# Optimization experiments

Measured on AMD Instinct MI355X. Metric: run time of the kernel, lower is better.

## Reference

```python
import jax, jax.numpy as jnp
import numpy as np

FC = 8  # heads_count
EPS = 1e-12  # torch F.normalize eps


def setup_inputs() -> dict:
    key = jax.random.key(0)
    ks = jax.random.split(key, 8)
    n, l, s, C, H = 4, 4096, 256, 256, 256
    return {
        "x0": jax.random.normal(ks[0], (n, l, C), jnp.float32),
        "center1": jax.random.normal(ks[1], (n, s, C), jnp.float32),
        "W0": jax.random.normal(ks[2], (H, C), jnp.float32) * 0.05,
        "b0": jax.random.normal(ks[3], (H,), jnp.float32) * 0.05,
        "W1": jax.random.normal(ks[4], (2 * H, C), jnp.float32) * 0.05,
        "b1": jax.random.normal(ks[5], (2 * H,), jnp.float32) * 0.05,
        "Wm": jax.random.normal(ks[6], (C, H), jnp.float32) * 0.05,
        "bm": jax.random.normal(ks[7], (C,), jnp.float32) * 0.05,
        "alpha": jnp.ones((1,), jnp.float32),
        "beta": jnp.zeros((1,), jnp.float32),
    }


def _l2norm(x):
    # matches torch F.normalize(dim=-1): x / max(||x||, eps)
    nrm = jnp.sqrt(jnp.sum(x * x, axis=-1, keepdims=True))
    return x / jnp.maximum(nrm, EPS)


def reference(x0, center1, W0, b0, W1, b1, Wm, bm, alpha, beta):
    n, l, c = x0.shape
    s = center1.shape[1]
    H = W0.shape[0]
    sc = H // FC
    m = n * FC
    # projections
    x0p = x0 @ W0.T + b0                        # [n, l, H]
    c1 = center1 @ W1.T + b1                    # [n, s, 2H]
    # split heads: 'n l (fc sc) -> (n fc) l sc'
    x0p = x0p.reshape(n, l, FC, sc).transpose(0, 2, 1, 3).reshape(m, l, sc)
    c1 = c1.reshape(n, s, FC, 2 * sc).transpose(0, 2, 1, 3).reshape(m, s, 2 * sc)
    c_point, c_value = c1[..., :sc], c1[..., sc:]
    # cosine similarity + affine + sigmoid
    sim = jnp.einsum('mlc,msc->mls', _l2norm(x0p), _l2norm(c_point))
    sim = jax.nn.sigmoid(alpha[0] * sim + beta[0])
    # top-1 hard routing
    max_vals = jnp.max(sim, axis=2)             # [m, l]
    max_idx = jnp.argmax(sim, axis=2)           # [m, l]
    gathered = jnp.take_along_axis(c_value, max_idx[:, :, None], axis=1)  # [m, l, sc]
    dispatched = max_vals[:, :, None] * gathered
    # '(n fc) l sc -> n l (fc sc)'
    dispatched = dispatched.reshape(n, FC, l, sc).transpose(0, 2, 1, 3).reshape(n, l, H)
    return dispatched @ Wm.T + bm               # [n, l, c]
```

## Files before the change

### kernel.cpp

```cpp
#include <hip/hip_runtime.h>
#include <math.h>

#define Nn 4
#define Ll 4096
#define Ss 256
#define Cc 256
#define FC 8
#define SC 32

typedef __attribute__((ext_vector_type(8))) short short8;
typedef __attribute__((ext_vector_type(8))) _Float16 half8;
typedef __attribute__((ext_vector_type(4))) float f32x4;

__device__ __forceinline__ unsigned short f2bf(float x) {
  unsigned int u = __float_as_uint(x);
  return (unsigned short)((u + 0x7FFFu + ((u >> 16) & 1u)) >> 16);
}

__device__ __forceinline__ void split8v(float4 a, float4 b,
                                        half8& hi, half8& lo) {
  float v[8] = {a.x, a.y, a.z, a.w, b.x, b.y, b.z, b.w};
#pragma unroll
  for (int i = 0; i < 8; i++) {
    float x = v[i];
    _Float16 h = (_Float16)x;
    float r = (x - (float)h) * 2048.f;
    hi[i] = h;
    lo[i] = (_Float16)r;
  }
}

#define STAGE(Abuf, Bbuf, K0)                                               \
  {                                                                         \
    _Pragma("unroll")                                                       \
    for (int j = 0; j < 4; j++) {                                           \
      int c = wave * 4 + j;                                                 \
      const float* g = Ag + (m0blk + 8 * c + lr) * Cc + (K0) + scol;        \
      __builtin_amdgcn_global_load_lds(                                     \
          (const __attribute__((address_space(1))) void*)g,                 \
          (__attribute__((address_space(3))) void*)((Abuf) + c * 256),      \
          16, 0, 0);                                                        \
    }                                                                       \
    _Pragma("unroll")                                                       \
    for (int j = 0; j < 2; j++) {                                           \
      int c = wave * 2 + j;                                                 \
      const float* g =                                                      \
          Bg + (size_t)(n0blk + 8 * c + lr) * Cc + (K0) + scol;             \
      __builtin_amdgcn_global_load_lds(                                     \
          (const __attribute__((address_space(1))) void*)g,                 \
          (__attribute__((address_space(3))) void*)((Bbuf) + c * 256),      \
          16, 0, 0);                                                        \
    }                                                                       \
  }

#define KSTEP(Ac, Bc)                                                       \
  {                                                                         \
    half8 Bh[2], Bl[2];                                                     \
    _Pragma("unroll")                                                       \
    for (int ni = 0; ni < 2; ni++) {                                        \
      int rw = bR0 + ni * 16 + l15;                                         \
      int rb = rw * 32, xs = rw & 7;                                        \
      float4 f0 = *(const float4*)&(Bc)[rb + (((quad * 2) ^ xs) << 2)];     \
      float4 f1 = *(const float4*)&(Bc)[rb + (((quad * 2 + 1) ^ xs) << 2)]; \
      split8v(f0, f1, Bh[ni], Bl[ni]);                                      \
    }                                                                       \
    _Pragma("unroll")                                                       \
    for (int mi = 0; mi < 4; mi++) {                                        \
      int rw = aR0 + mi * 16 + l15;                                         \
      int rb = rw * 32, xs = rw & 7;                                        \
      float4 f0 = *(const float4*)&(Ac)[rb + (((quad * 2) ^ xs) << 2)];     \
      float4 f1 = *(const float4*)&(Ac)[rb + (((quad * 2 + 1) ^ xs) << 2)]; \
      half8 Ah, Al;                                                         \
      split8v(f0, f1, Ah, Al);                                              \
      _Pragma("unroll")                                                     \
      for (int ni = 0; ni < 2; ni++) {                                      \
        acc1[mi][ni] = __builtin_amdgcn_mfma_f32_16x16x32_f16(              \
            Ah, Bh[ni], acc1[mi][ni], 0, 0, 0);                             \
        acc2[mi][ni] = __builtin_amdgcn_mfma_f32_16x16x32_f16(              \
            Ah, Bl[ni], acc2[mi][ni], 0, 0, 0);                             \
        acc2[mi][ni] = __builtin_amdgcn_mfma_f32_16x16x32_f16(              \
            Al, Bh[ni], acc2[mi][ni], 0, 0, 0);                             \
      }                                                                     \
    }                                                                       \
  }

__global__ __launch_bounds__(256) void proj_mfma_k(
    const float* __restrict__ x0, const float* __restrict__ W0,
    const float* __restrict__ b0, const float* __restrict__ center1,
    const float* __restrict__ W1, const float* __restrict__ b1,
    float* __restrict__ xn, float* __restrict__ cpn, float* __restrict__ cval) {
  __shared__ float As[2][128 * 32];
  __shared__ float Bs[2][64 * 32];
  int t = threadIdx.x;
  int wave = t >> 6, lane = t & 63;
  int quad = lane >> 4, l15 = lane & 15;
  int l8 = lane & 7, lr = lane >> 3;
  int scol = (l8 ^ lr) << 2;
  int b = blockIdx.x;

  const float *Ag, *Bg, *bias;
  size_t m0blk;
  int n0blk;
  bool isX = (b < 512);
  if (isX) {
    int rt = b & 127, cb = b >> 7;
    m0blk = (size_t)rt * 128;
    n0blk = cb * 64;
    Ag = x0; Bg = W0; bias = b0;
  } else {
    int b2 = b - 512;
    m0blk = (size_t)(b2 >> 3) * 128;
    n0blk = (b2 & 7) * 64;
    Ag = center1; Bg = W1; bias = b1;
  }

  int n0w = n0blk + (wave >> 1) * 32;
  int aR0 = (wave & 1) * 64;
  int bR0 = (wave >> 1) * 32;

  f32x4 acc1[4][2], acc2[4][2];
#pragma unroll
  for (int ni = 0; ni < 2; ni++) {
    float bv = bias[n0w + ni * 16 + l15];
    f32x4 ci = {bv, bv, bv, bv};
    f32x4 zz = {0.f, 0.f, 0.f, 0.f};
#pragma unroll
    for (int mi = 0; mi < 4; mi++) { acc1[mi][ni] = ci; acc2[mi][ni] = zz; }
  }

  float* Ac = &As[0][0]; float* An = &As[1][0];
  float* Bc = &Bs[0][0]; float* Bn = &Bs[1][0];
  STAGE(Ac, Bc, 0);
#pragma unroll 1
  for (int kt = 0; kt < 8; kt++) {
    if (kt < 7) {
      STAGE(An, Bn, (kt + 1) * 32);
      asm volatile("s_waitcnt vmcnt(6)" ::: "memory");
    } else {
      asm volatile("s_waitcnt vmcnt(0)" ::: "memory");
    }
    __builtin_amdgcn_sched_barrier(0);
    __syncthreads();
    KSTEP(Ac, Bc);
    __syncthreads();
    float* tp;
    tp = Ac; Ac = An; An = tp;
    tp = Bc; Bc = Bn; Bn = tp;
  }

  if (isX) {
    size_t m0 = m0blk + aR0;
#pragma unroll
    for (int mi = 0; mi < 4; mi++) {
#pragma unroll
      for (int reg = 0; reg < 4; reg++) {
        size_t row = m0 + mi * 16 + quad * 4 + reg;
        float* orow = xn + row * Cc + n0w;
#pragma unroll
        for (int ni = 0; ni < 2; ni++)
          orow[ni * 16 + l15] =
              acc1[mi][ni][reg] + acc2[mi][ni][reg] * (1.f / 2048.f);
      }
    }
  } else {
    int f = n0w >> 6;
    bool point = (n0w & 32) == 0;
    int m0 = (int)m0blk + aR0;
#pragma unroll
    for (int mi = 0; mi < 4; mi++) {
#pragma unroll
      for (int reg = 0; reg < 4; reg++) {
        int row = m0 + mi * 16 + quad * 4 + reg;
        int nI = row >> 8, s = row & 255;
        float v0 = acc1[mi][0][reg] + acc2[mi][0][reg] * (1.f / 2048.f);
        float v1 = acc1[mi][1][reg] + acc2[mi][1][reg] * (1.f / 2048.f);
        size_t base = (((size_t)nI * FC + f) * Ss + s) * SC;
        if (point) {
          float ss = v0 * v0 + v1 * v1;
          ss += __shfl_xor(ss, 1, 64);
          ss += __shfl_xor(ss, 2, 64);
          ss += __shfl_xor(ss, 4, 64);
          ss += __shfl_xor(ss, 8, 64);
          float rin = 1.f / fmaxf(sqrtf(ss), 1e-12f);
          cpn[base + l15] = v0 * rin;
          cpn[base + 16 + l15] = v1 * rin;
        } else {
          cval[base + l15] = v0;
          cval[base + 16 + l15] = v1;
        }
      }
    }
  }
}

__global__ __launch_bounds__(256) void sim_k(
    float* __restrict__ xn, const float* __restrict__ cpn,
    const float* __restrict__ cval, const float* __restrict__ alphap,
    const float* __restrict__ betap) {
  __shared__ half8 BhS[4][256];
  __shared__ half8 BlS[4][256];
  int t = threadIdx.x;
  int wave = t >> 6, lane = t & 63;
  int quad = lane >> 4, l15 = lane & 15;
  int lt = blockIdx.x & 63;
  int nf = blockIdx.x >> 6;
  int f = nf & 7, nI = nf >> 3;
  int l0 = lt * 64;
  const float* cp = cpn + (size_t)nf * Ss * SC;

  {
    int s = t;
    float4 va[8];
#pragma unroll
    for (int q8 = 0; q8 < 8; q8++)
      va[q8] = *(const float4*)(cp + (size_t)s * SC + q8 * 4);
#pragma unroll
    for (int q = 0; q < 4; q++) {
      half8 h, l;
      split8v(va[2 * q], va[2 * q + 1], h, l);
      BhS[q][s] = h;
      BlS[q][s] = l;
    }
  }

  half8 Ah, Al;
  {
    const float* xrow =
        xn + ((size_t)nI * Ll + l0 + wave * 16 + l15) * Cc + f * SC + quad * 8;
    float4 a0 = *(const float4*)xrow;
    float4 a1 = *(const float4*)(xrow + 4);
    float ssq = a0.x * a0.x + a0.y * a0.y + a0.z * a0.z + a0.w * a0.w +
                a1.x * a1.x + a1.y * a1.y + a1.z * a1.z + a1.w * a1.w;
    ssq += __shfl_xor(ssq, 16, 64);
    ssq += __shfl_xor(ssq, 32, 64);
    float rin = 1.f / fmaxf(sqrtf(ssq), 1e-12f);
    a0.x *= rin; a0.y *= rin; a0.z *= rin; a0.w *= rin;
    a1.x *= rin; a1.y *= rin; a1.z *= rin; a1.w *= rin;
    split8v(a0, a1, Ah, Al);
  }

  __syncthreads();

  float a = alphap[0], bt = betap[0];
  float best[4];
  int bi[4];
#pragma unroll
  for (int r = 0; r < 4; r++) { best[r] = -3.0e38f; bi[r] = 0; }

#pragma unroll
  for (int j = 0; j < 16; j++) {
    half8 bh = BhS[quad][j * 16 + l15];
    half8 bl = BlS[quad][j * 16 + l15];
    f32x4 z = {0.f, 0.f, 0.f, 0.f};
    f32x4 c1 = __builtin_amdgcn_mfma_f32_16x16x32_f16(Ah, bh, z, 0, 0, 0);
    f32x4 c2 = __builtin_amdgcn_mfma_f32_16x16x32_f16(Ah, bl, z, 0, 0, 0);
    c2 = __builtin_amdgcn_mfma_f32_16x16x32_f16(Al, bh, c2, 0, 0, 0);
    int s = j * 16 + l15;
#pragma unroll
    for (int r = 0; r < 4; r++) {
      float v = c1[r] + c2[r] * (1.f / 2048.f);
      float tv = fmaf(a, v, bt);
      if (tv > best[r]) { best[r] = tv; bi[r] = s; }
    }
  }

#pragma unroll
  for (int r = 0; r < 4; r++) {
    float bv = best[r];
    int ix = bi[r];
#pragma unroll
    for (int m = 1; m <= 8; m <<= 1) {
      float ov = __shfl_xor(bv, m, 64);
      int oi = __shfl_xor(ix, m, 64);
      if (ov > bv || (ov == bv && oi < ix)) { bv = ov; ix = oi; }
    }
    float mv = 1.f / (1.f + expf(-bv));
    const float* cvp = cval + ((size_t)nf * Ss + ix) * SC;
    float* orow =
        xn + ((size_t)nI * Ll + l0 + wave * 16 + quad * 4 + r) * Cc + f * SC;
    orow[l15] = cvp[l15] * mv;
    orow[l15 + 16] = cvp[l15 + 16] * mv;
  }
}

__global__ __launch_bounds__(256) void out_mfma_k(
    const float* __restrict__ xn, const float* __restrict__ Wm,
    const float* __restrict__ bm, float* __restrict__ out) {
  int t = threadIdx.x;
  int wave = t >> 6, lane = t & 63;
  int quad = lane >> 4, l15 = lane & 15;
  size_t m0 = (size_t)(blockIdx.x >> 1) * 128 + (wave & 1) * 64;
  int n0 = (blockIdx.x & 1) * 128 + (wave >> 1) * 64;

  f32x4 acc[4][4];
#pragma unroll
  for (int ni = 0; ni < 4; ni++) {
    float bv = bm[n0 + ni * 16 + l15];
    f32x4 ci = {bv, bv, bv, bv};
#pragma unroll
    for (int mi = 0; mi < 4; mi++) acc[mi][ni] = ci;
  }

  for (int kt = 0; kt < 8; kt++) {
    int k0 = kt * 32 + quad * 8;
    short8 Af[4], Bf[4];
#pragma unroll
    for (int mi = 0; mi < 4; mi++) {
      const float* p = xn + (m0 + mi * 16 + l15) * Cc + k0;
      float4 lo = *(const float4*)p;
      float4 hi = *(const float4*)(p + 4);
      short8 fr;
      fr[0] = (short)f2bf(lo.x); fr[1] = (short)f2bf(lo.y);
      fr[2] = (short)f2bf(lo.z); fr[3] = (short)f2bf(lo.w);
      fr[4] = (short)f2bf(hi.x); fr[5] = (short)f2bf(hi.y);
      fr[6] = (short)f2bf(hi.z); fr[7] = (short)f2bf(hi.w);
      Af[mi] = fr;
    }
#pragma unroll
    for (int ni = 0; ni < 4; ni++) {
      const float* p = Wm + (size_t)(n0 + ni * 16 + l15) * Cc + k0;
      float4 lo = *(const float4*)p;
      float4 hi = *(const float4*)(p + 4);
      short8 fr;
      fr[0] = (short)f2bf(lo.x); fr[1] = (short)f2bf(lo.y);
      fr[2] = (short)f2bf(lo.z); fr[3] = (short)f2bf(lo.w);
      fr[4] = (short)f2bf(hi.x); fr[5] = (short)f2bf(hi.y);
      fr[6] = (short)f2bf(hi.z); fr[7] = (short)f2bf(hi.w);
      Bf[ni] = fr;
    }
#pragma unroll
    for (int mi = 0; mi < 4; mi++)
#pragma unroll
      for (int ni = 0; ni < 4; ni++)
        acc[mi][ni] = __builtin_amdgcn_mfma_f32_16x16x32_bf16(
            Af[mi], Bf[ni], acc[mi][ni], 0, 0, 0);
  }

#pragma unroll
  for (int mi = 0; mi < 4; mi++) {
#pragma unroll
    for (int reg = 0; reg < 4; reg++) {
      size_t row = m0 + mi * 16 + quad * 4 + reg;
      float* orow = out + row * Cc + n0;
#pragma unroll
      for (int ni = 0; ni < 4; ni++)
        orow[ni * 16 + l15] = acc[mi][ni][reg];
    }
  }
}

extern "C" void kernel_launch(void* const* d_in, const int* in_sizes, int n_in,
                              void* d_out, int out_size, void* d_ws, size_t ws_size,
                              hipStream_t stream) {
  const float* x0      = (const float*)d_in[0];
  const float* center1 = (const float*)d_in[1];
  const float* W0      = (const float*)d_in[2];
  const float* b0      = (const float*)d_in[3];
  const float* W1      = (const float*)d_in[4];
  const float* b1      = (const float*)d_in[5];
  const float* Wm      = (const float*)d_in[6];
  const float* bm      = (const float*)d_in[7];
  const float* alpha   = (const float*)d_in[8];
  const float* beta    = (const float*)d_in[9];
  float* out = (float*)d_out;
  float* ws  = (float*)d_ws;

  float* xn   = ws;
  float* cpn  = xn + (size_t)Nn * Ll * Cc;
  float* cval = cpn + (size_t)Nn * FC * Ss * SC;

  proj_mfma_k<<<dim3(576), dim3(256), 0, stream>>>(
      x0, W0, b0, center1, W1, b1, xn, cpn, cval);
  sim_k<<<dim3(32 * 64), dim3(256), 0, stream>>>(xn, cpn, cval, alpha, beta);
  out_mfma_k<<<dim3(256), dim3(256), 0, stream>>>(xn, Wm, bm, out);
}
```

Baseline: 149.5 us.

## Load projection GEMM operands directly from global memory, dropping LDS staging

```diff
diff --git a/kernel.cpp b/kernel.cpp
--- a/kernel.cpp
+++ b/kernel.cpp
@@ -30,72 +30,14 @@
   }
 }
 
-#define STAGE(Abuf, Bbuf, K0)                                               \
-  {                                                                         \
-    _Pragma("unroll")                                                       \
-    for (int j = 0; j < 4; j++) {                                           \
-      int c = wave * 4 + j;                                                 \
-      const float* g = Ag + (m0blk + 8 * c + lr) * Cc + (K0) + scol;        \
-      __builtin_amdgcn_global_load_lds(                                     \
-          (const __attribute__((address_space(1))) void*)g,                 \
-          (__attribute__((address_space(3))) void*)((Abuf) + c * 256),      \
-          16, 0, 0);                                                        \
-    }                                                                       \
-    _Pragma("unroll")                                                       \
-    for (int j = 0; j < 2; j++) {                                           \
-      int c = wave * 2 + j;                                                 \
-      const float* g =                                                      \
-          Bg + (size_t)(n0blk + 8 * c + lr) * Cc + (K0) + scol;             \
-      __builtin_amdgcn_global_load_lds(                                     \
-          (const __attribute__((address_space(1))) void*)g,                 \
-          (__attribute__((address_space(3))) void*)((Bbuf) + c * 256),      \
-          16, 0, 0);                                                        \
-    }                                                                       \
-  }
-
-#define KSTEP(Ac, Bc)                                                       \
-  {                                                                         \
-    half8 Bh[2], Bl[2];                                                     \
-    _Pragma("unroll")                                                       \
-    for (int ni = 0; ni < 2; ni++) {                                        \
-      int rw = bR0 + ni * 16 + l15;                                         \
-      int rb = rw * 32, xs = rw & 7;                                        \
-      float4 f0 = *(const float4*)&(Bc)[rb + (((quad * 2) ^ xs) << 2)];     \
-      float4 f1 = *(const float4*)&(Bc)[rb + (((quad * 2 + 1) ^ xs) << 2)]; \
-      split8v(f0, f1, Bh[ni], Bl[ni]);                                      \
-    }                                                                       \
-    _Pragma("unroll")                                                       \
-    for (int mi = 0; mi < 4; mi++) {                                        \
-      int rw = aR0 + mi * 16 + l15;                                         \
-      int rb = rw * 32, xs = rw & 7;                                        \
-      float4 f0 = *(const float4*)&(Ac)[rb + (((quad * 2) ^ xs) << 2)];     \
-      float4 f1 = *(const float4*)&(Ac)[rb + (((quad * 2 + 1) ^ xs) << 2)]; \
-      half8 Ah, Al;                                                         \
-      split8v(f0, f1, Ah, Al);                                              \
-      _Pragma("unroll")                                                     \
-      for (int ni = 0; ni < 2; ni++) {                                      \
-        acc1[mi][ni] = __builtin_amdgcn_mfma_f32_16x16x32_f16(              \
-            Ah, Bh[ni], acc1[mi][ni], 0, 0, 0);                             \
-        acc2[mi][ni] = __builtin_amdgcn_mfma_f32_16x16x32_f16(              \
-            Ah, Bl[ni], acc2[mi][ni], 0, 0, 0);                             \
-        acc2[mi][ni] = __builtin_amdgcn_mfma_f32_16x16x32_f16(              \
-            Al, Bh[ni], acc2[mi][ni], 0, 0, 0);                             \
-      }                                                                     \
-    }                                                                       \
-  }
-
 __global__ __launch_bounds__(256) void proj_mfma_k(
     const float* __restrict__ x0, const float* __restrict__ W0,
     const float* __restrict__ b0, const float* __restrict__ center1,
     const float* __restrict__ W1, const float* __restrict__ b1,
     float* __restrict__ xn, float* __restrict__ cpn, float* __restrict__ cval) {
-  __shared__ float As[2][128 * 32];
-  __shared__ float Bs[2][64 * 32];
   int t = threadIdx.x;
   int wave = t >> 6, lane = t & 63;
   int quad = lane >> 4, l15 = lane & 15;
-  int l8 = lane & 7, lr = lane >> 3;
-  int scol = (l8 ^ lr) << 2;
   int b = blockIdx.x;
 
   const float *Ag, *Bg, *bias;
@@ -113,10 +55,8 @@
     n0blk = (b2 & 7) * 64;
     Ag = center1; Bg = W1; bias = b1;
   }
-
+  size_t m0 = m0blk + (size_t)(wave & 1) * 64;
   int n0w = n0blk + (wave >> 1) * 32;
-  int aR0 = (wave & 1) * 64;
-  int bR0 = (wave >> 1) * 32;
 
   f32x4 acc1[4][2], acc2[4][2];
 #pragma unroll
@@ -128,28 +68,34 @@
     for (int mi = 0; mi < 4; mi++) { acc1[mi][ni] = ci; acc2[mi][ni] = zz; }
   }
 
-  float* Ac = &As[0][0]; float* An = &As[1][0];
-  float* Bc = &Bs[0][0]; float* Bn = &Bs[1][0];
-  STAGE(Ac, Bc, 0);
-#pragma unroll 1
   for (int kt = 0; kt < 8; kt++) {
-    if (kt < 7) {
-      STAGE(An, Bn, (kt + 1) * 32);
-      asm volatile("s_waitcnt vmcnt(6)" ::: "memory");
-    } else {
-      asm volatile("s_waitcnt vmcnt(0)" ::: "memory");
-    }
-    __builtin_amdgcn_sched_barrier(0);
-    __syncthreads();
-    KSTEP(Ac, Bc);
-    __syncthreads();
-    float* tp;
-    tp = Ac; Ac = An; An = tp;
-    tp = Bc; Bc = Bn; Bn = tp;
+    int k0 = kt * 32 + quad * 8;
+    half8 Ah[4], Al[4];
+#pragma unroll
+    for (int mi = 0; mi < 4; mi++) {
+      const float* p = Ag + (m0 + mi * 16 + l15) * Cc + k0;
+      split8v(*(const float4*)p, *(const float4*)(p + 4), Ah[mi], Al[mi]);
+    }
+    half8 Bh[2], Bl[2];
+#pragma unroll
+    for (int ni = 0; ni < 2; ni++) {
+      const float* p = Bg + (size_t)(n0w + ni * 16 + l15) * Cc + k0;
+      split8v(*(const float4*)p, *(const float4*)(p + 4), Bh[ni], Bl[ni]);
+    }
+#pragma unroll
+    for (int mi = 0; mi < 4; mi++)
+#pragma unroll
+      for (int ni = 0; ni < 2; ni++) {
+        acc1[mi][ni] = __builtin_amdgcn_mfma_f32_16x16x32_f16(
+            Ah[mi], Bh[ni], acc1[mi][ni], 0, 0, 0);
+        acc2[mi][ni] = __builtin_amdgcn_mfma_f32_16x16x32_f16(
+            Ah[mi], Bl[ni], acc2[mi][ni], 0, 0, 0);
+        acc2[mi][ni] = __builtin_amdgcn_mfma_f32_16x16x32_f16(
+            Al[mi], Bh[ni], acc2[mi][ni], 0, 0, 0);
+      }
   }
 
   if (isX) {
-    size_t m0 = m0blk + aR0;
 #pragma unroll
     for (int mi = 0; mi < 4; mi++) {
 #pragma unroll
@@ -165,12 +111,11 @@
   } else {
     int f = n0w >> 6;
     bool point = (n0w & 32) == 0;
-    int m0 = (int)m0blk + aR0;
 #pragma unroll
     for (int mi = 0; mi < 4; mi++) {
 #pragma unroll
       for (int reg = 0; reg < 4; reg++) {
-        int row = m0 + mi * 16 + quad * 4 + reg;
+        int row = (int)m0 + mi * 16 + quad * 4 + reg;
         int nI = row >> 8, s = row & 255;
         float v0 = acc1[mi][0][reg] + acc2[mi][0][reg] * (1.f / 2048.f);
         float v1 = acc1[mi][1][reg] + acc2[mi][1][reg] * (1.f / 2048.f);
```

Measured after the change: 172.6 us. 15.5% more time.
